# Performance work log

Hardware: AMD Instinct MI355X
Metric: run time of the kernel (lower is better)

## Reference

```python
import jax, jax.numpy as jnp
import numpy as np

B, S, E, H, DK = 2, 2048, 2048, 16, 128


def _make_freq_pos_enc(dim, max_seq_len):
    # matches torch freq_pos_enc: interleaved repeat '(f r)' with r=2
    inv_freq = 1.0 / (10000.0 ** (jnp.arange(0, dim, 2, dtype=jnp.float32) / dim))
    pos = jnp.arange(max_seq_len, dtype=jnp.float32)
    pe = pos[:, None] * inv_freq[None, :]          # [S, dim/2]
    return jnp.repeat(pe, 2, axis=-1)              # [S, dim], interleaved


def setup_inputs() -> dict:
    key = jax.random.key(0)
    ks = jax.random.split(key, 5)
    sc = 1.0 / np.sqrt(E)
    return {
        "x": jax.random.normal(ks[0], (B, S, E), jnp.float32),
        "wq": jax.random.normal(ks[1], (H * DK, E), jnp.float32) * sc,
        "wk": jax.random.normal(ks[2], (H * DK, E), jnp.float32) * sc,
        "wv": jax.random.normal(ks[3], (H * DK, E), jnp.float32) * sc,
        "wo": jax.random.normal(ks[4], (E, H * DK), jnp.float32) * sc,
        "freq_pos_enc": _make_freq_pos_enc(DK, S),
        "num_heads": H,
        "d_k": DK,
    }


def rotate_half(u):
    # interleaved pairs: (d r) with r=2 -> (-u2, u1) interleaved back
    shp = u.shape
    u = u.reshape(shp[:-1] + (shp[-1] // 2, 2))
    u1, u2 = u[..., 0], u[..., 1]
    return jnp.stack((-u2, u1), axis=-1).reshape(shp)


def reference(x, wq, wk, wv, wo, freq_pos_enc, num_heads, d_k):
    b, s, _ = x.shape

    def proj(w):  # [B,S,E] @ [E, H*DK] -> [B,H,S,DK]
        return (x @ w.T).reshape(b, s, num_heads, d_k).transpose(0, 2, 1, 3)

    q, k, v = proj(wq), proj(wk), proj(wv)

    pe = freq_pos_enc[:s]                           # [S, DK]
    cos, sin = jnp.cos(pe), jnp.sin(pe)
    rot = lambda u: u * cos + rotate_half(u) * sin  # broadcast over [B,H]
    q, k = rot(q), rot(k)

    scale = 1.0 / jnp.sqrt(jnp.asarray(d_k, x.dtype))
    scores = jnp.einsum('bhqd,bhkd->bhqk', q, k) * scale
    causal = jnp.tril(jnp.ones((s, s), bool))
    scores = jnp.where(causal, scores, jnp.finfo(scores.dtype).min)
    attn = jnp.einsum('bhqk,bhkd->bhqd', jax.nn.softmax(scores, axis=-1), v)

    out = attn.transpose(0, 2, 1, 3).reshape(b, s, num_heads * d_k)
    return out @ wo.T
```

## Files before the change

kernel.cpp:

```cpp
#include <hip/hip_runtime.h>
#include <hip/hip_bf16.h>

typedef __attribute__((ext_vector_type(8))) short bf16x8;
typedef __attribute__((ext_vector_type(4))) float f32x4;
typedef unsigned short u16;
typedef unsigned int u32;

#define B_ 2
#define S_ 2048
#define E_ 2048
#define H_ 16
#define DK_ 128
#define SCALE_ 0.08838834764831845f
#define THR_RAW_ 90.5f

#define MFMA16(a,b,c) __builtin_amdgcn_mfma_f32_16x16x32_bf16((a),(b),(c),0,0,0)
#define GLD16(g, l) __builtin_amdgcn_global_load_lds((const __attribute__((address_space(1))) void*)(g), (__attribute__((address_space(3))) void*)(l), 16, 0, 0)

__device__ __forceinline__ float b2f(short s) {
    u32 u = ((u32)(u16)s) << 16;
    float f; __builtin_memcpy(&f, &u, 4); return f;
}

__global__ void cast_f32_bf16(const float* __restrict__ in, __hip_bfloat16* __restrict__ out, int n4) {
    int i = blockIdx.x * blockDim.x + threadIdx.x;
    if (i >= n4) return;
    float4 v = ((const float4*)in)[i];
    __hip_bfloat16 ob[4] = {__float2bfloat16(v.x), __float2bfloat16(v.y),
                            __float2bfloat16(v.z), __float2bfloat16(v.w)};
    ushort4 u; __builtin_memcpy(&u, ob, 8);
    ((ushort4*)out)[i] = u;
}

__global__ void cast_w4(const float* __restrict__ w0, const float* __restrict__ w1,
                        const float* __restrict__ w2, const float* __restrict__ w3,
                        __hip_bfloat16* __restrict__ o0, __hip_bfloat16* __restrict__ o1,
                        __hip_bfloat16* __restrict__ o2, __hip_bfloat16* __restrict__ o3,
                        int n4) {
    int i = blockIdx.x * blockDim.x + threadIdx.x;
    if (i >= n4) return;
    const float* in = blockIdx.y == 0 ? w0 : blockIdx.y == 1 ? w1 : blockIdx.y == 2 ? w2 : w3;
    __hip_bfloat16* out = blockIdx.y == 0 ? o0 : blockIdx.y == 1 ? o1 : blockIdx.y == 2 ? o2 : o3;
    float4 v = ((const float4*)in)[i];
    __hip_bfloat16 ob[4] = {__float2bfloat16(v.x), __float2bfloat16(v.y),
                            __float2bfloat16(v.z), __float2bfloat16(v.w)};
    ushort4 u; __builtin_memcpy(&u, ob, 8);
    ((ushort4*)out)[i] = u;
}

__global__ void trig_table(const float* __restrict__ pe, float* __restrict__ ct,
                           float* __restrict__ st) {
    int t = blockIdx.x * blockDim.x + threadIdx.x;
    int s = t >> 6, d2 = t & 63;
    float ang = pe[(size_t)s * DK_ + 2 * d2];
    ct[t] = cosf(ang);
    st[t] = sinf(ang);
}

__global__ __launch_bounds__(256, 2)
void gemm_qkv(const __hip_bfloat16* __restrict__ X,
              const __hip_bfloat16* __restrict__ WQ, const __hip_bfloat16* __restrict__ WK,
              const __hip_bfloat16* __restrict__ WV,
              __hip_bfloat16* __restrict__ Qo, __hip_bfloat16* __restrict__ Ko,
              __hip_bfloat16* __restrict__ Vo,
              const float* __restrict__ CT, const float* __restrict__ ST)
{
    __shared__ __align__(16) __hip_bfloat16 As[128 * 64];
    __shared__ __align__(16) __hip_bfloat16 Bs[128 * 64];
    const int tid = threadIdx.x;
    const int lane = tid & 63, wv = tid >> 6;
    const int wr = wv >> 1, wc = wv & 1;
    const int which = blockIdx.y >> 4;
    const __hip_bfloat16* W = which == 0 ? WQ : which == 1 ? WK : WV;
    const int m0 = blockIdx.x * 128, n0 = (blockIdx.y & 15) * 128;
    const int g = lane >> 4, c = lane & 15;
    const int K = E_;

    f32x4 acc[4][4];
    #pragma unroll
    for (int i = 0; i < 4; ++i)
        #pragma unroll
        for (int j = 0; j < 4; ++j) acc[i][j] = f32x4{0.f, 0.f, 0.f, 0.f};

    for (int k0 = 0; k0 < K; k0 += 64) {
        __syncthreads();
        #pragma unroll
        for (int it = 0; it < 4; ++it) {
            int o = (it * 256 + tid) * 16;
            int row = o >> 7;
            int colb = (o ^ ((row & 7) << 4)) & 127;
            GLD16((const char*)(X + (size_t)(m0 + row) * K + k0) + colb, (char*)As + o);
            GLD16((const char*)(W + (size_t)(n0 + row) * K + k0) + colb, (char*)Bs + o);
        }
        __syncthreads();
        #pragma unroll
        for (int ks = 0; ks < 2; ++ks) {
            bf16x8 af[4], bfm[4];
            #pragma unroll
            for (int i = 0; i < 4; ++i) {
                int arow = wr * 64 + i * 16 + c;
                int ab = arow * 128 + ((ks * 64 + g * 16) ^ ((arow & 7) << 4));
                af[i] = *(const bf16x8*)((const char*)As + ab);
                int brow = wc * 64 + i * 16 + c;
                int bb = brow * 128 + ((ks * 64 + g * 16) ^ ((brow & 7) << 4));
                bfm[i] = *(const bf16x8*)((const char*)Bs + bb);
            }
            #pragma unroll
            for (int i = 0; i < 4; ++i)
                #pragma unroll
                for (int j = 0; j < 4; ++j)
                    acc[i][j] = MFMA16(af[i], bfm[j], acc[i][j]);
        }
    }

    if (which < 2) {
        __hip_bfloat16* Cq = which == 0 ? Qo : Ko;
        #pragma unroll
        for (int i = 0; i < 4; ++i)
            #pragma unroll
            for (int j = 0; j < 4; ++j)
                #pragma unroll
                for (int r = 0; r < 4; ++r) {
                    float v = acc[i][j][r];
                    float vp = __shfl_xor(v, 1);
                    int m = m0 + wr * 64 + i * 16 + 4 * g + r;
                    int n = n0 + wc * 64 + j * 16 + c;
                    int srow = m & (S_ - 1), d = n & (DK_ - 1);
                    float cs = CT[srow * 64 + (d >> 1)];
                    float sn = ST[srow * 64 + (d >> 1)];
                    float o = (c & 1) ? __builtin_fmaf(v, cs, vp * sn)
                                      : __builtin_fmaf(v, cs, -vp * sn);
                    size_t a = ((size_t)((m >> 11) * 16 + (n >> 7)) * S_ + srow) * DK_ + d;
                    Cq[a] = __float2bfloat16(o);
                }
    } else {
        #pragma unroll
        for (int i = 0; i < 4; ++i)
            #pragma unroll
            for (int j = 0; j < 4; ++j) {
                int m = m0 + wr * 64 + i * 16 + 4 * g;
                int n = n0 + wc * 64 + j * 16 + c;
                int s0 = m & (S_ - 1), d = n & (DK_ - 1);
                __hip_bfloat16 ob[4];
                #pragma unroll
                for (int r = 0; r < 4; ++r) ob[r] = __float2bfloat16(acc[i][j][r]);
                ushort4 u; __builtin_memcpy(&u, ob, 8);
                size_t a = ((size_t)((m >> 11) * 16 + (n >> 7)) * DK_ + d) * S_ + s0;
                *(ushort4*)(Vo + a) = u;
            }
    }
}

__global__ __launch_bounds__(256, 2)
void gemm_out(const __hip_bfloat16* __restrict__ A, const __hip_bfloat16* __restrict__ W,
              float* __restrict__ Cout, int M, int N, int K)
{
    __shared__ __align__(16) __hip_bfloat16 As[128 * 64];
    __shared__ __align__(16) __hip_bfloat16 Bs[128 * 64];
    const int tid = threadIdx.x;
    const int lane = tid & 63, wv = tid >> 6;
    const int wr = wv >> 1, wc = wv & 1;
    const int m0 = blockIdx.x * 128, n0 = blockIdx.y * 128;
    const int g = lane >> 4, c = lane & 15;

    f32x4 acc[4][4];
    #pragma unroll
    for (int i = 0; i < 4; ++i)
        #pragma unroll
        for (int j = 0; j < 4; ++j) acc[i][j] = f32x4{0.f, 0.f, 0.f, 0.f};

    for (int k0 = 0; k0 < K; k0 += 64) {
        __syncthreads();
        #pragma unroll
        for (int it = 0; it < 4; ++it) {
            int o = (it * 256 + tid) * 16;
            int row = o >> 7;
            int colb = (o ^ ((row & 7) << 4)) & 127;
            GLD16((const char*)(A + (size_t)(m0 + row) * K + k0) + colb, (char*)As + o);
            GLD16((const char*)(W + (size_t)(n0 + row) * K + k0) + colb, (char*)Bs + o);
        }
        __syncthreads();
        #pragma unroll
        for (int ks = 0; ks < 2; ++ks) {
            bf16x8 af[4], bfm[4];
            #pragma unroll
            for (int i = 0; i < 4; ++i) {
                int arow = wr * 64 + i * 16 + c;
                int ab = arow * 128 + ((ks * 64 + g * 16) ^ ((arow & 7) << 4));
                af[i] = *(const bf16x8*)((const char*)As + ab);
                int brow = wc * 64 + i * 16 + c;
                int bb = brow * 128 + ((ks * 64 + g * 16) ^ ((brow & 7) << 4));
                bfm[i] = *(const bf16x8*)((const char*)Bs + bb);
            }
            #pragma unroll
            for (int i = 0; i < 4; ++i)
                #pragma unroll
                for (int j = 0; j < 4; ++j)
                    acc[i][j] = MFMA16(af[i], bfm[j], acc[i][j]);
        }
    }

    #pragma unroll
    for (int i = 0; i < 4; ++i)
        #pragma unroll
        for (int j = 0; j < 4; ++j)
            #pragma unroll
            for (int r = 0; r < 4; ++r) {
                int m = m0 + wr * 64 + i * 16 + 4 * g + r;
                int n = n0 + wc * 64 + j * 16 + c;
                Cout[(size_t)m * N + n] = acc[i][j][r];
            }
}

__device__ __forceinline__ void stage_kv(const __hip_bfloat16* Kp, const __hip_bfloat16* Vp,
                                         char* ks, char* vs, int kv0, int tid) {
    #pragma unroll
    for (int it = 0; it < 4; ++it) {
        int o = (it * 256 + tid) * 16;
        int row = o >> 8;
        int cb = (o ^ ((row & 7) << 4)) & 255;
        GLD16((const char*)(Kp + (size_t)(kv0 + row) * DK_) + cb, ks + o);
    }
    #pragma unroll
    for (int it = 0; it < 4; ++it) {
        int o = (it * 256 + tid) * 16;
        int row = o >> 7;
        int cb = (o ^ ((row & 7) << 4)) & 127;
        GLD16((const char*)(Vp + (size_t)row * S_ + kv0) + cb, vs + o);
    }
}

__global__ __launch_bounds__(256, 2)
void attn_kernel(const __hip_bfloat16* __restrict__ Q,
                 const __hip_bfloat16* __restrict__ Kt,
                 const __hip_bfloat16* __restrict__ VT,
                 __hip_bfloat16* __restrict__ O)
{
    __shared__ __align__(16) __hip_bfloat16 Ks[2][64 * 128];
    __shared__ __align__(16) __hip_bfloat16 Vs[2][128 * 64];
    __shared__ __align__(16) __hip_bfloat16 Ps[4][16 * 72];

    const int tid = threadIdx.x, lane = tid & 63, w = tid >> 6;
    const int g = lane >> 4, c = lane & 15;
    const int id = blockIdx.x;
    const int slot = id & 7, jj = id >> 3;
    const int bh = ((jj >> 4) << 3) | slot;
    const int xq = jj & 15;
    const int b = bh >> 4, h = bh & 15;
    const size_t base_bh = (size_t)bh * S_ * DK_;
    const __hip_bfloat16* Qp = Q + base_bh;
    const __hip_bfloat16* Kp = Kt + base_bh;
    const __hip_bfloat16* Vp = VT + base_bh;

    #pragma unroll 1
    for (int pass = 0; pass < 2; ++pass) {
        const int qt = pass ? (31 - xq) : xq;
        const int qw = qt * 64 + w * 16;
        const int ntiles = qt + 1;

        bf16x8 qf[4];
        #pragma unroll
        for (int ds = 0; ds < 4; ++ds)
            qf[ds] = *(const bf16x8*)(Qp + (size_t)(qw + c) * DK_ + ds * 32 + g * 8);

        f32x4 oacc[8];
        #pragma unroll
        for (int fd = 0; fd < 8; ++fd) oacc[fd] = f32x4{0.f, 0.f, 0.f, 0.f};
        float M[4], L[4];
        #pragma unroll
        for (int r = 0; r < 4; ++r) { M[r] = -1e30f; L[r] = 0.f; }

        stage_kv(Kp, Vp, (char*)Ks[0], (char*)Vs[0], 0, tid);
        __syncthreads();

        int cur = 0;
        for (int t = 0; t < ntiles; ++t) {
            const int kv0 = t * 64;
            if (t + 1 < ntiles)
                stage_kv(Kp, Vp, (char*)Ks[cur ^ 1], (char*)Vs[cur ^ 1], kv0 + 64, tid);

            const bool diag = (kv0 + 63 > qw);

            f32x4 sacc[4];
            #pragma unroll
            for (int f = 0; f < 4; ++f) sacc[f] = f32x4{0.f, 0.f, 0.f, 0.f};
            #pragma unroll
            for (int f = 0; f < 4; ++f) {
                #pragma unroll
                for (int ds = 0; ds < 4; ++ds) {
                    int krow = f * 16 + c;
                    int kbyt = krow * 256 + ((ds * 64 + g * 16) ^ ((krow & 7) << 4));
                    bf16x8 kf = *(const bf16x8*)((const char*)Ks[cur] + kbyt);
                    sacc[f] = MFMA16(qf[ds], kf, sacc[f]);
                }
            }

            float p[4][4];
            float mt[4] = {-1e30f, -1e30f, -1e30f, -1e30f};
            #pragma unroll
            for (int f = 0; f < 4; ++f)
                #pragma unroll
                for (int r = 0; r < 4; ++r) {
                    float v = sacc[f][r];
                    if (diag && (kv0 + f * 16 + c > qw + 4 * g + r)) v = -1e30f;
                    p[f][r] = v;
                    mt[r] = fmaxf(mt[r], v);
                }
            #pragma unroll
            for (int r = 0; r < 4; ++r) {
                float v = mt[r];
                v = fmaxf(v, __shfl_xor(v, 1));
                v = fmaxf(v, __shfl_xor(v, 2));
                v = fmaxf(v, __shfl_xor(v, 4));
                v = fmaxf(v, __shfl_xor(v, 8));
                mt[r] = v;
            }
            bool grow = (mt[0] > M[0] + THR_RAW_) || (mt[1] > M[1] + THR_RAW_) ||
                        (mt[2] > M[2] + THR_RAW_) || (mt[3] > M[3] + THR_RAW_);
            if (__any(grow)) {
                float al[4];
                #pragma unroll
                for (int r = 0; r < 4; ++r) {
                    float mn = fmaxf(M[r], mt[r]);
                    al[r] = __expf((M[r] - mn) * SCALE_);
                    M[r] = mn;
                    L[r] *= al[r];
                }
                #pragma unroll
                for (int fd = 0; fd < 8; ++fd)
                    #pragma unroll
                    for (int r = 0; r < 4; ++r) oacc[fd][r] *= al[r];
            }
            float ms[4];
            #pragma unroll
            for (int r = 0; r < 4; ++r) ms[r] = M[r] * SCALE_;
            float lt[4] = {0.f, 0.f, 0.f, 0.f};
            #pragma unroll
            for (int f = 0; f < 4; ++f)
                #pragma unroll
                for (int r = 0; r < 4; ++r) {
                    float e = __expf(__builtin_fmaf(p[f][r], SCALE_, -ms[r]));
                    lt[r] += e;
                    Ps[w][(4 * g + r) * 72 + f * 16 + c] = __float2bfloat16(e);
                }
            #pragma unroll
            for (int r = 0; r < 4; ++r) {
                float v = lt[r];
                v += __shfl_xor(v, 1);
                v += __shfl_xor(v, 2);
                v += __shfl_xor(v, 4);
                v += __shfl_xor(v, 8);
                L[r] += v;
            }

            #pragma unroll
            for (int ks2 = 0; ks2 < 2; ++ks2) {
                bf16x8 pf = *(const bf16x8*)&Ps[w][c * 72 + ks2 * 32 + g * 8];
                #pragma unroll
                for (int fd = 0; fd < 8; ++fd) {
                    int vrow = fd * 16 + c;
                    int vb = vrow * 128 + ((ks2 * 64 + g * 16) ^ ((vrow & 7) << 4));
                    bf16x8 vf = *(const bf16x8*)((const char*)Vs[cur] + vb);
                    oacc[fd] = MFMA16(pf, vf, oacc[fd]);
                }
            }
            __syncthreads();
            cur ^= 1;
        }

        float rl[4];
        #pragma unroll
        for (int r = 0; r < 4; ++r) rl[r] = 1.0f / L[r];
        #pragma unroll
        for (int fd = 0; fd < 8; ++fd) {
            #pragma unroll
            for (int r = 0; r < 4; ++r) {
                int s = qw + 4 * g + r;
                size_t a = ((size_t)(b * S_ + s)) * (H_ * DK_) + h * DK_ + fd * 16 + c;
                O[a] = __float2bfloat16(oacc[fd][r] * rl[r]);
            }
        }
    }
}

extern "C" void kernel_launch(void* const* d_in, const int* in_sizes, int n_in,
                              void* d_out, int out_size, void* d_ws, size_t ws_size,
                              hipStream_t stream) {
    const float* x  = (const float*)d_in[0];
    const float* wq = (const float*)d_in[1];
    const float* wk = (const float*)d_in[2];
    const float* wv = (const float*)d_in[3];
    const float* wo = (const float*)d_in[4];
    const float* pe = (const float*)d_in[5];
    float* out = (float*)d_out;

    const size_t XE = (size_t)B_ * S_ * E_;
    const size_t WE = (size_t)E_ * H_ * DK_;
    __hip_bfloat16* xb  = (__hip_bfloat16*)d_ws;
    __hip_bfloat16* wqb = xb + XE;
    __hip_bfloat16* wkb = wqb + WE;
    __hip_bfloat16* wvb = wkb + WE;
    __hip_bfloat16* wob = wvb + WE;
    __hip_bfloat16* qb  = wob + WE;
    __hip_bfloat16* kb  = qb + XE;
    __hip_bfloat16* vT  = kb + XE;
    __hip_bfloat16* at  = vT + XE;
    float* ct = (float*)(at + XE);
    float* st = ct + (size_t)S_ * 64;

    cast_f32_bf16<<<dim3((int)(XE / 4 / 256)), 256, 0, stream>>>(x, xb, (int)(XE / 4));
    cast_w4<<<dim3((int)(WE / 4 / 256), 4), 256, 0, stream>>>(wq, wk, wv, wo,
                                                              wqb, wkb, wvb, wob,
                                                              (int)(WE / 4));
    trig_table<<<dim3(S_ * 64 / 256), 256, 0, stream>>>(pe, ct, st);

    gemm_qkv<<<dim3(32, 48), 256, 0, stream>>>(xb, wqb, wkb, wvb, qb, kb, vT, ct, st);

    attn_kernel<<<dim3(512), 256, 0, stream>>>(qb, kb, vT, at);

    gemm_out<<<dim3(32, 16), 256, 0, stream>>>(at, wob, out, B_ * S_, E_, H_ * DK_);
}
```

Measured before the change: 273.4 us.

## Rewrite QKV GEMM as 256x256 eight-wave double-buffered pipelined kernel

Replaces the 128x128, 4-wave QKV projection GEMM with a 256x256 tile, 8-wave kernel that uses a K-step of 128, double-buffered LDS, and a four-phase schedule. Global-to-LDS loads for the next stages are issued between MFMA phases, with explicit vmcnt waits, s_barrier, and setprio to keep loads overlapped with compute. This aims to raise arithmetic intensity and hide memory latency. In exchange it uses 128KB of LDS per block, launches only 384 blocks on 256 CUs (tail imbalance), and carries a larger accumulator register footprint that limits occupancy.

```diff
diff --git a/kernel.cpp b/kernel.cpp
--- a/kernel.cpp
+++ b/kernel.cpp
@@ -57,74 +57,108 @@
     st[t] = sinf(ang);
 }
 
-__global__ __launch_bounds__(256, 2)
-void gemm_qkv(const __hip_bfloat16* __restrict__ X,
-              const __hip_bfloat16* __restrict__ WQ, const __hip_bfloat16* __restrict__ WK,
-              const __hip_bfloat16* __restrict__ WV,
-              __hip_bfloat16* __restrict__ Qo, __hip_bfloat16* __restrict__ Ko,
-              __hip_bfloat16* __restrict__ Vo,
-              const float* __restrict__ CT, const float* __restrict__ ST)
+
+#define STAGE_A8(BUF, MH, KB) do { \
+    _Pragma("unroll") for (int cc_ = 0; cc_ < 2; ++cc_) { \
+        int row_ = cc_*128 + (MH)*64 + (tid>>3); \
+        int gc_ = ((tid&7)*16) ^ ((row_&7)<<4); \
+        GLD16(Ab + (size_t)(m0+row_)*K2 + (KB) + gc_, \
+              (char*)As[BUF] + (cc_*128 + (MH)*64)*128 + tid*16); \
+    } } while (0)
+
+#define STAGE_B8(BUF, NH, KB) do { \
+    _Pragma("unroll") for (int cc_ = 0; cc_ < 2; ++cc_) { \
+        int rg_ = cc_*128 + ((tid>>8)<<6) + (NH)*32; \
+        int row_ = rg_ + ((tid&255)>>3); \
+        int gc_ = ((tid&7)*16) ^ ((row_&7)<<4); \
+        GLD16(Wb + (size_t)(n0+row_)*K2 + (KB) + gc_, \
+              (char*)Bs[BUF] + rg_*128 + (tid&255)*16); \
+    } } while (0)
+
+#define PHASE8(BUF, MH, NH, STAGE_STMT, TAIL_STMT) do { \
+    bf16x8 af_[4][2], bf_[2][2]; \
+    _Pragma("unroll") for (int i_ = 0; i_ < 4; ++i_) { \
+        int ar_ = wm*128 + ((MH)*4+i_)*16 + c; \
+        const char* ab_ = (const char*)As[BUF] + ar_*128; \
+        _Pragma("unroll") for (int ks_ = 0; ks_ < 2; ++ks_) \
+            af_[i_][ks_] = *(const bf16x8*)(ab_ + ((ks_*64 + g*16) ^ ((ar_&7)<<4))); \
+    } \
+    _Pragma("unroll") for (int j_ = 0; j_ < 2; ++j_) { \
+        int br_ = wn*64 + ((NH)*2+j_)*16 + c; \
+        const char* bb_ = (const char*)Bs[BUF] + br_*128; \
+        _Pragma("unroll") for (int ks_ = 0; ks_ < 2; ++ks_) \
+            bf_[j_][ks_] = *(const bf16x8*)(bb_ + ((ks_*64 + g*16) ^ ((br_&7)<<4))); \
+    } \
+    STAGE_STMT; \
+    __builtin_amdgcn_s_barrier(); \
+    asm volatile("s_waitcnt lgkmcnt(0)" ::: "memory"); \
+    __builtin_amdgcn_sched_barrier(0); \
+    __builtin_amdgcn_s_setprio(1); \
+    _Pragma("unroll") for (int i_ = 0; i_ < 4; ++i_) \
+        _Pragma("unroll") for (int j_ = 0; j_ < 2; ++j_) \
+            _Pragma("unroll") for (int ks_ = 0; ks_ < 2; ++ks_) \
+                acc[(MH)*4+i_][(NH)*2+j_] = MFMA16(af_[i_][ks_], bf_[j_][ks_], acc[(MH)*4+i_][(NH)*2+j_]); \
+    __builtin_amdgcn_s_setprio(0); \
+    TAIL_STMT; \
+    __builtin_amdgcn_s_barrier(); \
+} while (0)
+
+__global__ __launch_bounds__(512, 2)
+void gemm_qkv8(const __hip_bfloat16* __restrict__ X,
+               const __hip_bfloat16* __restrict__ WQ, const __hip_bfloat16* __restrict__ WK,
+               const __hip_bfloat16* __restrict__ WV,
+               __hip_bfloat16* __restrict__ Qo, __hip_bfloat16* __restrict__ Ko,
+               __hip_bfloat16* __restrict__ Vo,
+               const float* __restrict__ CT, const float* __restrict__ ST)
 {
-    __shared__ __align__(16) __hip_bfloat16 As[128 * 64];
-    __shared__ __align__(16) __hip_bfloat16 Bs[128 * 64];
-    const int tid = threadIdx.x;
-    const int lane = tid & 63, wv = tid >> 6;
-    const int wr = wv >> 1, wc = wv & 1;
-    const int which = blockIdx.y >> 4;
+    __shared__ __align__(16) __hip_bfloat16 As[2][256 * 64];
+    __shared__ __align__(16) __hip_bfloat16 Bs[2][256 * 64];
+    const int tid = threadIdx.x, lane = tid & 63, wid = tid >> 6;
+    const int wm = wid >> 2, wn = wid & 3;
+    const int g = (lane >> 4), c = lane & 15;
+    const int which = blockIdx.y >> 3;
     const __hip_bfloat16* W = which == 0 ? WQ : which == 1 ? WK : WV;
-    const int m0 = blockIdx.x * 128, n0 = (blockIdx.y & 15) * 128;
-    const int g = lane >> 4, c = lane & 15;
-    const int K = E_;
-
-    f32x4 acc[4][4];
+    const int m0 = blockIdx.x * 256, n0 = (blockIdx.y & 7) * 256;
+    const long K2 = E_ * 2;
+    const char* Ab = (const char*)X;
+    const char* Wb = (const char*)W;
+
+    f32x4 acc[8][4];
     #pragma unroll
-    for (int i = 0; i < 4; ++i)
+    for (int i = 0; i < 8; ++i)
         #pragma unroll
         for (int j = 0; j < 4; ++j) acc[i][j] = f32x4{0.f, 0.f, 0.f, 0.f};
 
-    for (int k0 = 0; k0 < K; k0 += 64) {
-        __syncthreads();
-        #pragma unroll
-        for (int it = 0; it < 4; ++it) {
-            int o = (it * 256 + tid) * 16;
-            int row = o >> 7;
-            int colb = (o ^ ((row & 7) << 4)) & 127;
-            GLD16((const char*)(X + (size_t)(m0 + row) * K + k0) + colb, (char*)As + o);
-            GLD16((const char*)(W + (size_t)(n0 + row) * K + k0) + colb, (char*)Bs + o);
-        }
-        __syncthreads();
-        #pragma unroll
-        for (int ks = 0; ks < 2; ++ks) {
-            bf16x8 af[4], bfm[4];
-            #pragma unroll
-            for (int i = 0; i < 4; ++i) {
-                int arow = wr * 64 + i * 16 + c;
-                int ab = arow * 128 + ((ks * 64 + g * 16) ^ ((arow & 7) << 4));
-                af[i] = *(const bf16x8*)((const char*)As + ab);
-                int brow = wc * 64 + i * 16 + c;
-                int bb = brow * 128 + ((ks * 64 + g * 16) ^ ((brow & 7) << 4));
-                bfm[i] = *(const bf16x8*)((const char*)Bs + bb);
-            }
-            #pragma unroll
-            for (int i = 0; i < 4; ++i)
-                #pragma unroll
-                for (int j = 0; j < 4; ++j)
-                    acc[i][j] = MFMA16(af[i], bfm[j], acc[i][j]);
-        }
+    STAGE_A8(0, 0, 0);  STAGE_B8(0, 0, 0);
+    STAGE_A8(0, 1, 0);  STAGE_B8(0, 1, 0);
+    STAGE_A8(1, 0, 128); STAGE_B8(1, 0, 128);
+    asm volatile("s_waitcnt vmcnt(4)" ::: "memory");
+    __builtin_amdgcn_s_barrier();
+
+    for (int t = 0; t < 32; ++t) {
+        const int buf = t & 1;
+        const long kb1 = (long)(t + 1) * 128;
+        const long kb2 = (long)(t + 2) * 128;
+        PHASE8(buf, 0, 0, { if (t < 31) STAGE_A8(buf ^ 1, 1, kb1); }, {});
+        PHASE8(buf, 0, 1, { if (t < 31) STAGE_B8(buf ^ 1, 1, kb1); }, {});
+        PHASE8(buf, 1, 0, { if (t < 30) STAGE_A8(buf, 0, kb2); }, {});
+        PHASE8(buf, 1, 1, { if (t < 30) STAGE_B8(buf, 0, kb2); },
+               { if (t < 30) { asm volatile("s_waitcnt vmcnt(4)" ::: "memory"); }
+                 else if (t == 30) { asm volatile("s_waitcnt vmcnt(0)" ::: "memory"); } });
     }
 
     if (which < 2) {
         __hip_bfloat16* Cq = which == 0 ? Qo : Ko;
         #pragma unroll
-        for (int i = 0; i < 4; ++i)
-            #pragma unroll
-            for (int j = 0; j < 4; ++j)
+        for (int mi = 0; mi < 8; ++mi)
+            #pragma unroll
+            for (int nj = 0; nj < 4; ++nj)
                 #pragma unroll
                 for (int r = 0; r < 4; ++r) {
-                    float v = acc[i][j][r];
+                    float v = acc[mi][nj][r];
                     float vp = __shfl_xor(v, 1);
-                    int m = m0 + wr * 64 + i * 16 + 4 * g + r;
-                    int n = n0 + wc * 64 + j * 16 + c;
+                    int m = m0 + wm * 128 + mi * 16 + 4 * g + r;
+                    int n = n0 + wn * 64 + nj * 16 + c;
                     int srow = m & (S_ - 1), d = n & (DK_ - 1);
                     float cs = CT[srow * 64 + (d >> 1)];
                     float sn = ST[srow * 64 + (d >> 1)];
@@ -135,15 +169,15 @@
                 }
     } else {
         #pragma unroll
-        for (int i = 0; i < 4; ++i)
-            #pragma unroll
-            for (int j = 0; j < 4; ++j) {
-                int m = m0 + wr * 64 + i * 16 + 4 * g;
-                int n = n0 + wc * 64 + j * 16 + c;
+        for (int mi = 0; mi < 8; ++mi)
+            #pragma unroll
+            for (int nj = 0; nj < 4; ++nj) {
+                int m = m0 + wm * 128 + mi * 16 + 4 * g;
+                int n = n0 + wn * 64 + nj * 16 + c;
                 int s0 = m & (S_ - 1), d = n & (DK_ - 1);
                 __hip_bfloat16 ob[4];
                 #pragma unroll
-                for (int r = 0; r < 4; ++r) ob[r] = __float2bfloat16(acc[i][j][r]);
+                for (int r = 0; r < 4; ++r) ob[r] = __float2bfloat16(acc[mi][nj][r]);
                 ushort4 u; __builtin_memcpy(&u, ob, 8);
                 size_t a = ((size_t)((m >> 11) * 16 + (n >> 7)) * DK_ + d) * S_ + s0;
                 *(ushort4*)(Vo + a) = u;
@@ -414,7 +448,7 @@
                                                               (int)(WE / 4));
     trig_table<<<dim3(S_ * 64 / 256), 256, 0, stream>>>(pe, ct, st);
 
-    gemm_qkv<<<dim3(32, 48), 256, 0, stream>>>(xb, wqb, wkb, wvb, qb, kb, vT, ct, st);
+    gemm_qkv8<<<dim3(16, 24), 512, 0, stream>>>(xb, wqb, wkb, wvb, qb, kb, vT, ct, st);
 
     attn_kernel<<<dim3(512), 256, 0, stream>>>(qb, kb, vT, at);
 
```

After: 298.0 us. 1.09x slower.

## Rewrite QKV GEMM as 8-wave 256x192 double-buffered pipelined kernel

Applied to the files above, without the earlier changes.

Replaces the 128x128 single-buffered QKV projection GEMM with a 512-thread kernel over 256x192 tiles of a concatenated Q/K/V weight matrix. The new kernel double-buffers LDS, splits each K-step into four MFMA phases interleaved with async global-to-LDS loads, and raises wave priority with setprio around MFMA bursts. It also remaps block indices for L2 locality. The aim is to hide load latency and raise MFMA utilisation. In exchange, LDS use and register pressure go up, and the epilogue needs more branching for tiles that straddle the Q/K/V boundaries.

```diff
diff --git a/kernel.cpp b/kernel.cpp
--- a/kernel.cpp
+++ b/kernel.cpp
@@ -57,97 +57,196 @@
     st[t] = sinf(ang);
 }
 
-__global__ __launch_bounds__(256, 2)
-void gemm_qkv(const __hip_bfloat16* __restrict__ X,
-              const __hip_bfloat16* __restrict__ WQ, const __hip_bfloat16* __restrict__ WK,
-              const __hip_bfloat16* __restrict__ WV,
-              __hip_bfloat16* __restrict__ Qo, __hip_bfloat16* __restrict__ Ko,
-              __hip_bfloat16* __restrict__ Vo,
-              const float* __restrict__ CT, const float* __restrict__ ST)
+
+#define ST_B(BUF, Q, KB) do { \
+    int row_ = (Q) * 64 + (tid >> 3); \
+    int gc_ = ((tid & 7) * 16) ^ ((row_ & 7) << 4); \
+    GLD16(Wb + (size_t)(n0 + row_) * K2 + (KB) + gc_, (char*)Bs[BUF] + (Q) * 8192 + tid * 16); \
+} while (0)
+
+#define ST_A(BUF, Q, KB) do { \
+    int row_ = (Q) * 64 + (tid >> 3); \
+    int gc_ = ((tid & 7) * 16) ^ ((row_ & 7) << 4); \
+    GLD16(Ab + (size_t)(m0 + row_) * K2 + (KB) + gc_, (char*)As[BUF] + (Q) * 8192 + tid * 16); \
+} while (0)
+
+#define WAIT_MFMA_ENTER() do { \
+    __builtin_amdgcn_s_barrier(); \
+    asm volatile("s_waitcnt lgkmcnt(0)" ::: "memory"); \
+    __builtin_amdgcn_sched_barrier(0); \
+    __builtin_amdgcn_s_setprio(1); \
+} while (0)
+
+__global__ __launch_bounds__(512, 2)
+void gemm_qkv8(const __hip_bfloat16* __restrict__ X,
+               const __hip_bfloat16* __restrict__ Wcat,
+               __hip_bfloat16* __restrict__ Qo, __hip_bfloat16* __restrict__ Ko,
+               __hip_bfloat16* __restrict__ Vo,
+               const float* __restrict__ CT, const float* __restrict__ ST)
 {
-    __shared__ __align__(16) __hip_bfloat16 As[128 * 64];
-    __shared__ __align__(16) __hip_bfloat16 Bs[128 * 64];
-    const int tid = threadIdx.x;
-    const int lane = tid & 63, wv = tid >> 6;
-    const int wr = wv >> 1, wc = wv & 1;
-    const int which = blockIdx.y >> 4;
-    const __hip_bfloat16* W = which == 0 ? WQ : which == 1 ? WK : WV;
-    const int m0 = blockIdx.x * 128, n0 = (blockIdx.y & 15) * 128;
+    __shared__ __align__(16) __hip_bfloat16 As[2][256 * 64];
+    __shared__ __align__(16) __hip_bfloat16 Bs[2][192 * 64];
+    const int tid = threadIdx.x, lane = tid & 63, wid = tid >> 6;
+    const int wm = wid >> 2, wn = wid & 3;
     const int g = lane >> 4, c = lane & 15;
-    const int K = E_;
-
-    f32x4 acc[4][4];
+    const int raw = blockIdx.x;
+    const int wg = (raw & 7) * 64 + (raw >> 3);
+    const int mtile = wg & 15, ntile = wg >> 4;
+    const int m0 = mtile * 256, n0 = ntile * 192;
+    const long K2 = E_ * 2;
+    const char* Ab = (const char*)X;
+    const char* Wb = (const char*)Wcat;
+
+    f32x4 acc[8][3];
     #pragma unroll
-    for (int i = 0; i < 4; ++i)
-        #pragma unroll
-        for (int j = 0; j < 4; ++j) acc[i][j] = f32x4{0.f, 0.f, 0.f, 0.f};
-
-    for (int k0 = 0; k0 < K; k0 += 64) {
-        __syncthreads();
-        #pragma unroll
-        for (int it = 0; it < 4; ++it) {
-            int o = (it * 256 + tid) * 16;
-            int row = o >> 7;
-            int colb = (o ^ ((row & 7) << 4)) & 127;
-            GLD16((const char*)(X + (size_t)(m0 + row) * K + k0) + colb, (char*)As + o);
-            GLD16((const char*)(W + (size_t)(n0 + row) * K + k0) + colb, (char*)Bs + o);
-        }
-        __syncthreads();
-        #pragma unroll
-        for (int ks = 0; ks < 2; ++ks) {
-            bf16x8 af[4], bfm[4];
-            #pragma unroll
-            for (int i = 0; i < 4; ++i) {
-                int arow = wr * 64 + i * 16 + c;
-                int ab = arow * 128 + ((ks * 64 + g * 16) ^ ((arow & 7) << 4));
-                af[i] = *(const bf16x8*)((const char*)As + ab);
-                int brow = wc * 64 + i * 16 + c;
-                int bb = brow * 128 + ((ks * 64 + g * 16) ^ ((brow & 7) << 4));
-                bfm[i] = *(const bf16x8*)((const char*)Bs + bb);
-            }
-            #pragma unroll
-            for (int i = 0; i < 4; ++i)
-                #pragma unroll
-                for (int j = 0; j < 4; ++j)
-                    acc[i][j] = MFMA16(af[i], bfm[j], acc[i][j]);
-        }
+    for (int i = 0; i < 8; ++i)
+        #pragma unroll
+        for (int j = 0; j < 3; ++j) acc[i][j] = f32x4{0.f, 0.f, 0.f, 0.f};
+
+    bf16x8 af[4][2], b01[2][2], b2[2];
+
+    ST_B(0, 0, 0); ST_B(0, 1, 0); ST_B(0, 2, 0);
+    ST_A(0, 0, 0); ST_A(0, 2, 0);
+    ST_A(0, 1, 0); ST_A(0, 3, 0);
+    asm volatile("s_waitcnt vmcnt(2)" ::: "memory");
+    __builtin_amdgcn_s_barrier();
+
+    #pragma unroll 1
+    for (int t = 0; t < 32; ++t) {
+        const int buf = t & 1;
+        const long kb1 = (long)(t + 1) * 128;
+        const char* Ac = (const char*)As[buf];
+        const char* Bc = (const char*)Bs[buf];
+
+        #pragma unroll
+        for (int i = 0; i < 4; ++i) {
+            int ar = wm * 128 + i * 16 + c;
+            const char* ab = Ac + ar * 128;
+            af[i][0] = *(const bf16x8*)(ab + ((g * 16) ^ ((ar & 7) << 4)));
+            af[i][1] = *(const bf16x8*)(ab + ((64 + g * 16) ^ ((ar & 7) << 4)));
+        }
+        #pragma unroll
+        for (int nj = 0; nj < 2; ++nj) {
+            int br = wn * 48 + nj * 16 + c;
+            const char* bb = Bc + br * 128;
+            b01[nj][0] = *(const bf16x8*)(bb + ((g * 16) ^ ((br & 7) << 4)));
+            b01[nj][1] = *(const bf16x8*)(bb + ((64 + g * 16) ^ ((br & 7) << 4)));
+        }
+        if (t < 31) { ST_B(buf ^ 1, 0, kb1); ST_B(buf ^ 1, 1, kb1); ST_B(buf ^ 1, 2, kb1); }
+        WAIT_MFMA_ENTER();
+        #pragma unroll
+        for (int i = 0; i < 4; ++i)
+            #pragma unroll
+            for (int nj = 0; nj < 2; ++nj)
+                #pragma unroll
+                for (int k = 0; k < 2; ++k)
+                    acc[i][nj] = MFMA16(af[i][k], b01[nj][k], acc[i][nj]);
+        __builtin_amdgcn_s_setprio(0);
+        __builtin_amdgcn_s_barrier();
+
+        {
+            int br = wn * 48 + 32 + c;
+            const char* bb = Bc + br * 128;
+            b2[0] = *(const bf16x8*)(bb + ((g * 16) ^ ((br & 7) << 4)));
+            b2[1] = *(const bf16x8*)(bb + ((64 + g * 16) ^ ((br & 7) << 4)));
+        }
+        if (t < 31) { ST_A(buf ^ 1, 0, kb1); ST_A(buf ^ 1, 2, kb1); }
+        WAIT_MFMA_ENTER();
+        #pragma unroll
+        for (int i = 0; i < 4; ++i)
+            #pragma unroll
+            for (int k = 0; k < 2; ++k)
+                acc[i][2] = MFMA16(af[i][k], b2[k], acc[i][2]);
+        __builtin_amdgcn_s_setprio(0);
+        if (t < 31) { asm volatile("s_waitcnt vmcnt(5)" ::: "memory"); }
+        else        { asm volatile("s_waitcnt vmcnt(0)" ::: "memory"); }
+        __builtin_amdgcn_s_barrier();
+
+        #pragma unroll
+        for (int i = 0; i < 4; ++i) {
+            int ar = wm * 128 + 64 + i * 16 + c;
+            const char* ab = Ac + ar * 128;
+            af[i][0] = *(const bf16x8*)(ab + ((g * 16) ^ ((ar & 7) << 4)));
+            af[i][1] = *(const bf16x8*)(ab + ((64 + g * 16) ^ ((ar & 7) << 4)));
+        }
+        if (t < 31) { ST_A(buf ^ 1, 1, kb1); ST_A(buf ^ 1, 3, kb1); }
+        WAIT_MFMA_ENTER();
+        #pragma unroll
+        for (int i = 0; i < 4; ++i)
+            #pragma unroll
+            for (int nj = 0; nj < 2; ++nj)
+                #pragma unroll
+                for (int k = 0; k < 2; ++k)
+                    acc[4 + i][nj] = MFMA16(af[i][k], b01[nj][k], acc[4 + i][nj]);
+        __builtin_amdgcn_s_setprio(0);
+        __builtin_amdgcn_s_barrier();
+
+        __builtin_amdgcn_s_setprio(1);
+        #pragma unroll
+        for (int i = 0; i < 4; ++i)
+            #pragma unroll
+            for (int k = 0; k < 2; ++k)
+                acc[4 + i][2] = MFMA16(af[i][k], b2[k], acc[4 + i][2]);
+        __builtin_amdgcn_s_setprio(0);
+        if (t < 31) { asm volatile("s_waitcnt vmcnt(2)" ::: "memory"); }
+        __builtin_amdgcn_s_barrier();
     }
 
-    if (which < 2) {
-        __hip_bfloat16* Cq = which == 0 ? Qo : Ko;
-        #pragma unroll
-        for (int i = 0; i < 4; ++i)
-            #pragma unroll
-            for (int j = 0; j < 4; ++j)
+    #pragma unroll
+    for (int mi = 0; mi < 8; ++mi) {
+        #pragma unroll
+        for (int nj = 0; nj < 3; ++nj) {
+            const int nbase = n0 + wn * 48 + nj * 16;
+            const int t0 = nbase >> 11, t1 = (nbase + 15) >> 11;
+            const int m_r0 = m0 + wm * 128 + mi * 16 + 4 * g;
+            const int bb = m_r0 >> 11;
+            if (t0 == 2 && t1 == 2) {
+                const int n = nbase + c, d = n & (DK_ - 1), h = (n >> 7) & 15;
+                const int s0 = m_r0 & (S_ - 1);
+                __hip_bfloat16 ob[4];
+                #pragma unroll
+                for (int r = 0; r < 4; ++r) ob[r] = __float2bfloat16(acc[mi][nj][r]);
+                ushort4 u; __builtin_memcpy(&u, ob, 8);
+                size_t a = ((size_t)(bb * 16 + h) * DK_ + d) * S_ + s0;
+                *(ushort4*)(Vo + a) = u;
+            } else if (t1 < 2) {
+                __hip_bfloat16* Cq = (t0 == 0) ? Qo : Ko;
+                const int n = nbase + c, d = n & (DK_ - 1), h = (n >> 7) & 15;
                 #pragma unroll
                 for (int r = 0; r < 4; ++r) {
-                    float v = acc[i][j][r];
+                    float v = acc[mi][nj][r];
                     float vp = __shfl_xor(v, 1);
-                    int m = m0 + wr * 64 + i * 16 + 4 * g + r;
-                    int n = n0 + wc * 64 + j * 16 + c;
-                    int srow = m & (S_ - 1), d = n & (DK_ - 1);
+                    int srow = (m_r0 + r) & (S_ - 1);
                     float cs = CT[srow * 64 + (d >> 1)];
                     float sn = ST[srow * 64 + (d >> 1)];
                     float o = (c & 1) ? __builtin_fmaf(v, cs, vp * sn)
                                       : __builtin_fmaf(v, cs, -vp * sn);
-                    size_t a = ((size_t)((m >> 11) * 16 + (n >> 7)) * S_ + srow) * DK_ + d;
+                    size_t a = ((size_t)(bb * 16 + h) * S_ + srow) * DK_ + d;
                     Cq[a] = __float2bfloat16(o);
                 }
-    } else {
-        #pragma unroll
-        for (int i = 0; i < 4; ++i)
-            #pragma unroll
-            for (int j = 0; j < 4; ++j) {
-                int m = m0 + wr * 64 + i * 16 + 4 * g;
-                int n = n0 + wc * 64 + j * 16 + c;
-                int s0 = m & (S_ - 1), d = n & (DK_ - 1);
-                __hip_bfloat16 ob[4];
-                #pragma unroll
-                for (int r = 0; r < 4; ++r) ob[r] = __float2bfloat16(acc[i][j][r]);
-                ushort4 u; __builtin_memcpy(&u, ob, 8);
-                size_t a = ((size_t)((m >> 11) * 16 + (n >> 7)) * DK_ + d) * S_ + s0;
-                *(ushort4*)(Vo + a) = u;
-            }
+            } else {
+                const int n = nbase + c, tens = n >> 11;
+                const int rn = n & 2047, d = rn & (DK_ - 1), h = rn >> 7;
+                #pragma unroll
+                for (int r = 0; r < 4; ++r) {
+                    float v = acc[mi][nj][r];
+                    float vp = __shfl_xor(v, 1);
+                    int srow = (m_r0 + r) & (S_ - 1);
+                    if (tens == 2) {
+                        size_t a = ((size_t)(bb * 16 + h) * DK_ + d) * S_ + srow;
+                        Vo[a] = __float2bfloat16(v);
+                    } else {
+                        __hip_bfloat16* Cq = (tens == 0) ? Qo : Ko;
+                        float cs = CT[srow * 64 + (d >> 1)];
+                        float sn = ST[srow * 64 + (d >> 1)];
+                        float o = (c & 1) ? __builtin_fmaf(v, cs, vp * sn)
+                                          : __builtin_fmaf(v, cs, -vp * sn);
+                        size_t a = ((size_t)(bb * 16 + h) * S_ + srow) * DK_ + d;
+                        Cq[a] = __float2bfloat16(o);
+                    }
+                }
+            }
+        }
     }
 }
 
@@ -414,7 +513,7 @@
                                                               (int)(WE / 4));
     trig_table<<<dim3(S_ * 64 / 256), 256, 0, stream>>>(pe, ct, st);
 
-    gemm_qkv<<<dim3(32, 48), 256, 0, stream>>>(xb, wqb, wkb, wvb, qb, kb, vT, ct, st);
+    gemm_qkv8<<<dim3(512), 512, 0, stream>>>(xb, wqb, qb, kb, vT, ct, st);
 
     attn_kernel<<<dim3(512), 256, 0, stream>>>(qb, kb, vT, at);
 
```

Measured after the change: 267.6 us. 1.02x faster.
